# Optimization experiments

Hardware: AMD Instinct MI355X
Metric: run time of the kernel (lower is better)

Reference implementation:

```python
import jax, jax.numpy as jnp
import numpy as np

B, N, K = 8, 1024, 16        # graphs, points per graph, kNN fan-in (loop=True includes self)
LATENT = 256
EPS = 1e-5                   # PyG BatchNorm eps


def _bn(x, g, b):
    # training-mode batch norm over all leading (node/edge) dims, per channel
    ax = tuple(range(x.ndim - 1))
    mu = jnp.mean(x, axis=ax, keepdims=True)
    var = jnp.var(x, axis=ax, keepdims=True)
    return g * (x - mu) * jax.lax.rsqrt(var + EPS) + b


def setup_inputs() -> dict:
    key = jax.random.key(0)
    ks = jax.random.split(key, 12)

    def lin(k, fi, fo):
        s = (6.0 / (fi + fo)) ** 0.5
        kw, kb = jax.random.split(k)
        W = jax.random.uniform(kw, (fi, fo), jnp.float32, -s, s)
        bb = jax.random.uniform(kb, (fo,), jnp.float32, -s, s)
        return W, bb

    pos = jax.random.normal(ks[0], (B * N, 3), jnp.float32)
    batch = jnp.repeat(jnp.arange(B, dtype=jnp.int32), N)

    c1_W1, c1_b1 = lin(ks[1], 6, 64)
    c1_W2, c1_b2 = lin(ks[2], 64, 64)
    c2_W1, c2_b1 = lin(ks[3], 67, 64)
    c2_W2, c2_b2 = lin(ks[4], 64, 128)
    c2_W3, c2_b3 = lin(ks[5], 128, 1024)
    lin_W, lin_b = lin(ks[6], 1024, LATENT)

    return {
        "pos": pos, "batch": batch,
        "c1_W1": c1_W1, "c1_b1": c1_b1,
        "c1_g1": jnp.ones((64,), jnp.float32), "c1_be1": jnp.zeros((64,), jnp.float32),
        "c1_W2": c1_W2, "c1_b2": c1_b2,
        "c2_W1": c2_W1, "c2_b1": c2_b1,
        "c2_g1": jnp.ones((64,), jnp.float32), "c2_be1": jnp.zeros((64,), jnp.float32),
        "c2_W2": c2_W2, "c2_b2": c2_b2,
        "c2_g2": jnp.ones((128,), jnp.float32), "c2_be2": jnp.zeros((128,), jnp.float32),
        "c2_W3": c2_W3, "c2_b3": c2_b3,
        "lin_W": lin_W, "lin_b": lin_b,
        "lin_g": jnp.ones((LATENT,), jnp.float32), "lin_be": jnp.zeros((LATENT,), jnp.float32),
    }


def reference(pos, batch,
              c1_W1, c1_b1, c1_g1, c1_be1, c1_W2, c1_b2,
              c2_W1, c2_b1, c2_g1, c2_be1, c2_W2, c2_b2,
              c2_g2, c2_be2, c2_W3, c2_b3,
              lin_W, lin_b, lin_g, lin_be):
    # ---- kNN graph (per-graph, loop=True: self is nearest) ----
    p3 = pos.reshape(B, N, 3)
    sq = jnp.sum(p3 * p3, axis=-1)                                   # [B,N]
    d = sq[:, :, None] + sq[:, None, :] - 2.0 * jnp.einsum('bnd,bmd->bnm', p3, p3)
    _, nbr = jax.lax.top_k(-d, K)                                    # [B,N,K] neighbor ids
    idx = (nbr + (jnp.arange(B) * N)[:, None, None]).reshape(B * N, K)

    # ---- PointNetConv 1: gather -> MLP([6,64,64]) -> max aggregate ----
    pj = pos[idx]                                                    # [P,K,3]
    rel = pj - pos[:, None, :]                                       # [P,K,3]
    feat = jnp.concatenate([pj, rel], axis=-1)                       # [P,K,6]
    h = jax.nn.relu(_bn(feat @ c1_W1 + c1_b1, c1_g1, c1_be1))
    x1 = jnp.max(h @ c1_W2 + c1_b2, axis=1)                          # [P,64]

    # ---- PointNetConv 2: MLP([67,64,128,1024]) -> max aggregate ----
    feat2 = jnp.concatenate([x1[idx], rel], axis=-1)                 # [P,K,67]
    h = jax.nn.relu(_bn(feat2 @ c2_W1 + c2_b1, c2_g1, c2_be1))
    h = jax.nn.relu(_bn(h @ c2_W2 + c2_b2, c2_g2, c2_be2))
    x2 = jnp.max(h @ c2_W3 + c2_b3, axis=1)                          # [P,1024]

    # ---- global max pool per graph + final MLP (plain_last=False) ----
    g = x2.reshape(B, N, -1).max(axis=1)                             # [B,1024]
    return jax.nn.relu(_bn(g @ lin_W + lin_b, lin_g, lin_be))        # [B,LATENT]
```

## Files before the change

### kernel.cpp

```cpp
#include <hip/hip_runtime.h>
#include <math.h>

#define NB   8
#define NPTS 1024
#define PTS  8192
#define KNN  16
#define PK   (PTS*KNN)

typedef __attribute__((ext_vector_type(8))) _Float16 f16x8;
typedef __attribute__((ext_vector_type(4))) float f32x4;

__device__ __forceinline__ unsigned short f2h(float f) {
  _Float16 h = (_Float16)f;
  union { _Float16 h; unsigned short u; } c; c.h = h;
  return c.u;
}
__device__ __forceinline__ float h2f(unsigned short u) {
  union { unsigned short u; _Float16 h; } c; c.u = u;
  return (float)c.h;
}
__device__ __forceinline__ int lanerank(unsigned long long m) {
  return __builtin_amdgcn_mbcnt_hi((unsigned)(m >> 32),
         __builtin_amdgcn_mbcnt_lo((unsigned)m, 0));
}

__global__ __launch_bounds__(256) void knn_conv1_kernel(const float* __restrict__ pos,
    const float* __restrict__ W1, const float* __restrict__ b1,
    int* __restrict__ idx, float* __restrict__ rel,
    unsigned short* __restrict__ z1h, float* __restrict__ mid1) {
  __shared__ float px[NPTS], py[NPTS], pz[NPTS];
  __shared__ float feat[4][KNN][6];
  __shared__ float ls[256], ls2[256];
  const int t = threadIdx.x;
  const int wv = t >> 6, lane = t & 63;
  const int b = blockIdx.x;
  const int graph = b >> 8;
  const int base = graph << 10;
  for (int j = t; j < NPTS; j += 256) {
    px[j] = pos[3*(base+j)];
    py[j] = pos[3*(base+j)+1];
    pz[j] = pos[3*(base+j)+2];
  }
  __syncthreads();

  const int il = ((b & 255) << 2) + wv;
  const int i  = base + il;
  const float pix = px[il], piy = py[il], piz = pz[il];
  const float sqi = pix*pix + piy*piy + piz*piz;

  unsigned key[16];
  #pragma unroll
  for (int q = 0; q < 16; ++q) {
    const int j = (q << 6) + lane;
    const float x = px[j], y = py[j], z = pz[j];
    const float sqj = x*x + y*y + z*z;
    const float dt  = pix*x + piy*y + piz*z;
    const float d   = sqi + sqj - 2.0f*dt;
    const unsigned db = __float_as_uint(d);
    key[q] = (db >> 31) ? ~db : (db | 0x80000000u);
  }

  unsigned V = 0;
  #pragma unroll 1
  for (int bb = 31; bb >= 0; --bb) {
    const unsigned test = V | (1u << bb);
    int cnt = 0;
    #pragma unroll
    for (int q = 0; q < 16; ++q)
      cnt += __popcll(__ballot(key[q] < test));
    if (cnt < 16) V = test;
  }

  int c = 0;
  #pragma unroll
  for (int q = 0; q < 16; ++q)
    c += __popcll(__ballot(key[q] < V));

  int p_lt = 0, p_eq = c;
  #pragma unroll 1
  for (int q = 0; q < 16; ++q) {
    const unsigned long long mlt = __ballot(key[q] < V);
    const unsigned long long meq = __ballot(key[q] == V);
    int slot = -1;
    if (key[q] < V) slot = p_lt + lanerank(mlt);
    else if (key[q] == V) {
      const int s = p_eq + lanerank(meq);
      if (s < 16) slot = s;
    }
    if (slot >= 0) {
      const int j = (q << 6) + lane;
      const int r = i*KNN + slot;
      const float rx = px[j] - pix, ry = py[j] - piy, rz = pz[j] - piz;
      idx[r] = base + j;
      rel[3*r] = rx; rel[3*r+1] = ry; rel[3*r+2] = rz;
      feat[wv][slot][0] = px[j]; feat[wv][slot][1] = py[j]; feat[wv][slot][2] = pz[j];
      feat[wv][slot][3] = rx;    feat[wv][slot][4] = ry;    feat[wv][slot][5] = rz;
    }
    p_lt += __popcll(mlt);
    p_eq += __popcll(meq);
  }

  float w[6];
  #pragma unroll
  for (int q = 0; q < 6; ++q) w[q] = W1[q*64 + lane];
  const float bbv = b1[lane];
  float s = 0.0f, s2 = 0.0f;
  #pragma unroll
  for (int k = 0; k < KNN; ++k) {
    float z = bbv;
    #pragma unroll
    for (int q = 0; q < 6; ++q) z += feat[wv][k][q]*w[q];
    z1h[(size_t)(i*KNN + k)*64 + lane] = f2h(z);
    s += z; s2 += z*z;
  }
  ls[t] = s; ls2[t] = s2;
  __syncthreads();
  if (t < 64) {
    float a  = ls[t] + ls[t+64] + ls[t+128] + ls[t+192];
    float a2 = ls2[t] + ls2[t+64] + ls2[t+128] + ls2[t+192];
    const int cp = (b & 7) * 128;
    atomicAdd(&mid1[cp + t], a);
    atomicAdd(&mid1[cp + 64 + t], a2);
  }
}

__global__ __launch_bounds__(256) void wprep_kernel(const float* __restrict__ W3,
    const float* __restrict__ W2, const float* __restrict__ W1c2,
    const float* __restrict__ W2c1,
    unsigned short* __restrict__ W3T, unsigned short* __restrict__ W2T,
    unsigned short* __restrict__ w1T, unsigned short* __restrict__ W2c1T,
    float* __restrict__ mids) {
  const int b = blockIdx.x, t = threadIdx.x;
  if (b < 128) {
    const int k = b;
    const int ks = k >> 5, qd = (k >> 3) & 3, e = k & 7;
    for (int n = t; n < 1024; n += 256) {
      const int nb = n >> 4, mc = n & 15;
      W3T[((nb*4 + ks) << 9) + qd*128 + mc*8 + e] = f2h(W3[(size_t)k*1024 + n]);
    }
  } else if (b < 132) {
    for (int id = (b-128)*2048 + t; id < (b-127)*2048; id += 256) {
      const int n = id >> 6, k = id & 63;
      W2T[n*64 + k] = f2h(W2[k*128 + n]);
    }
  } else if (b < 136) {
    for (int id = (b-132)*1024 + t; id < (b-131)*1024; id += 256) {
      const int n = id >> 6, k = id & 63;
      w1T[n*64 + k] = f2h(W1c2[k*64 + n]);
    }
  } else if (b < 140) {
    for (int id = (b-136)*1024 + t; id < (b-135)*1024; id += 256) {
      const int n = id >> 6, k = id & 63;
      W2c1T[n*64 + k] = f2h(W2c1[k*64 + n]);
    }
  } else {
    for (int i2 = t; i2 < 4096; i2 += 256) mids[i2] = 0.0f;
  }
}

__global__ __launch_bounds__(256) void conv1_l2max_mfma(
    const unsigned short* __restrict__ z1h, const float* __restrict__ mid1,
    const float* __restrict__ g1, const float* __restrict__ be1,
    const unsigned short* __restrict__ W2T, const float* __restrict__ b2,
    unsigned short* __restrict__ x1h) {
  __shared__ unsigned short As[128*64];
  __shared__ float scl[64], shl[64];
  const int r0 = blockIdx.x * 128;
  const int t = threadIdx.x;
  const int lane = t & 63, w = t >> 6;
  const int quad = lane >> 4, mcol = lane & 15;
  const float invR = 1.0f / (float)PK;

  if (t < 64) {
    float s = 0.0f, s2 = 0.0f;
    #pragma unroll
    for (int k = 0; k < 8; ++k) { s += mid1[k*128 + t]; s2 += mid1[k*128 + 64 + t]; }
    const float mu  = s * invR;
    const float var = s2 * invR - mu*mu;
    const float sc  = g1[t] * rsqrtf(var + 1e-5f);
    scl[t] = sc; shl[t] = be1[t] - mu*sc;
  }
  __syncthreads();

  {
    const int kb = t & 7, rr = t >> 3;
    float sc[8], sh[8];
    #pragma unroll
    for (int q = 0; q < 8; ++q) { sc[q] = scl[kb*8 + q]; sh[q] = shl[kb*8 + q]; }
    #pragma unroll
    for (int it = 0; it < 4; ++it) {
      const int r = rr + it*32;
      union { uint4 v; unsigned short s[8]; } in;
      in.v = *(const uint4*)(z1h + (size_t)(r0 + r)*64 + kb*8);
      union { unsigned short s[8]; uint4 v; } o;
      #pragma unroll
      for (int q = 0; q < 8; ++q)
        o.s[q] = f2h(fmaxf(h2f(in.s[q])*sc[q] + sh[q], 0.0f));
      *(uint4*)(As + r*64 + ((kb ^ (r & 7)) * 8)) = o.v;
    }
  }
  __syncthreads();

  const int wrow = (w >> 1) * 64;
  const int wncol = (w & 1) * 32;

  f32x4 acc[4][2];
  #pragma unroll
  for (int mi = 0; mi < 4; ++mi)
    #pragma unroll
    for (int ni = 0; ni < 2; ++ni)
      acc[mi][ni] = (f32x4){0.f, 0.f, 0.f, 0.f};

  #pragma unroll
  for (int ks = 0; ks < 2; ++ks) {
    f16x8 af[4], bfr[2];
    #pragma unroll
    for (int mi = 0; mi < 4; ++mi) {
      const int row = wrow + mi*16 + mcol;
      af[mi] = *(const f16x8*)(As + row*64 + (((ks*4 + quad) ^ (row & 7)) * 8));
    }
    #pragma unroll
    for (int ni = 0; ni < 2; ++ni) {
      const int nr = wncol + ni*16 + mcol;
      bfr[ni] = *(const f16x8*)(W2T + nr*64 + ks*32 + quad*8);
    }
    #pragma unroll
    for (int mi = 0; mi < 4; ++mi)
      #pragma unroll
      for (int ni = 0; ni < 2; ++ni)
        acc[mi][ni] = __builtin_amdgcn_mfma_f32_16x16x32_f16(af[mi], bfr[ni], acc[mi][ni], 0, 0, 0);
  }

  float bb[2];
  #pragma unroll
  for (int ni = 0; ni < 2; ++ni) bb[ni] = b2[wncol + ni*16 + mcol];
  #pragma unroll
  for (int mi = 0; mi < 4; ++mi) {
    const int p = blockIdx.x*8 + (w >> 1)*4 + mi;
    #pragma unroll
    for (int ni = 0; ni < 2; ++ni) {
      f32x4 a = acc[mi][ni];
      float m = fmaxf(fmaxf(a[0], a[1]), fmaxf(a[2], a[3]));
      m = fmaxf(m, __shfl_xor(m, 16));
      m = fmaxf(m, __shfl_xor(m, 32));
      if (quad == 0) x1h[(size_t)p*64 + wncol + ni*16 + mcol] = f2h(m + bb[ni]);
    }
  }
}

__global__ __launch_bounds__(256) void conv2_l1_mfma(
    const unsigned short* __restrict__ x1h, const int* __restrict__ idx,
    const float* __restrict__ rel, const unsigned short* __restrict__ w1T,
    const float* __restrict__ W1full, const float* __restrict__ b1,
    unsigned short* __restrict__ zah, float* __restrict__ midA) {
  __shared__ unsigned short S[128*64];
  __shared__ int   idxr[128];
  __shared__ float rl[128*3];
  __shared__ float ps[256];
  const int r0 = blockIdx.x * 128;
  const int t = threadIdx.x;
  const int lane = t & 63, w = t >> 6;
  const int quad = lane >> 4, mcol = lane & 15;

  if (t < 128) idxr[t] = idx[r0 + t];
  else if (t < 224) *(float4*)(rl + (t-128)*4) = *(const float4*)(rel + (size_t)r0*3 + (t-128)*4);
  __syncthreads();

  {
    const int kb = t & 7, rr = t >> 3;
    #pragma unroll
    for (int it = 0; it < 4; ++it) {
      const int r = rr + it*32;
      const int gj = idxr[r];
      const uint4 v = *(const uint4*)(x1h + (size_t)gj*64 + kb*8);
      *(uint4*)(S + r*64 + ((kb ^ (r & 7)) * 8)) = v;
    }
  }
  __syncthreads();

  const int wrow = (w >> 1) * 64;
  const int wcol = (w & 1) * 32;

  f16x8 af[2][4], bfr[2][2];
  #pragma unroll
  for (int ks = 0; ks < 2; ++ks)
    #pragma unroll
    for (int mi = 0; mi < 4; ++mi) {
      const int row = wrow + mi*16 + mcol;
      af[ks][mi] = *(const f16x8*)(S + row*64 + (((ks*4 + quad) ^ (row & 7)) * 8));
    }
  #pragma unroll
  for (int ks = 0; ks < 2; ++ks)
    #pragma unroll
    for (int ni = 0; ni < 2; ++ni) {
      const int nr = wcol + ni*16 + mcol;
      bfr[ks][ni] = *(const f16x8*)(w1T + nr*64 + ks*32 + quad*8);
    }

  f32x4 acc[4][2];
  #pragma unroll
  for (int mi = 0; mi < 4; ++mi)
    #pragma unroll
    for (int ni = 0; ni < 2; ++ni)
      acc[mi][ni] = (f32x4){0.f, 0.f, 0.f, 0.f};

  #pragma unroll
  for (int ks = 0; ks < 2; ++ks)
    #pragma unroll
    for (int mi = 0; mi < 4; ++mi)
      #pragma unroll
      for (int ni = 0; ni < 2; ++ni)
        acc[mi][ni] = __builtin_amdgcn_mfma_f32_16x16x32_f16(af[ks][mi], bfr[ks][ni], acc[mi][ni], 0, 0, 0);

  __syncthreads();

  float bb[2], wr0[2], wr1[2], wr2[2];
  #pragma unroll
  for (int ni = 0; ni < 2; ++ni) {
    const int col = wcol + ni*16 + mcol;
    bb[ni]  = b1[col];
    wr0[ni] = W1full[64*64 + col];
    wr1[ni] = W1full[65*64 + col];
    wr2[ni] = W1full[66*64 + col];
  }
  float s[2] = {0,0}, s2[2] = {0,0};
  #pragma unroll
  for (int mi = 0; mi < 4; ++mi) {
    #pragma unroll
    for (int j = 0; j < 4; ++j) {
      const int row = wrow + mi*16 + quad*4 + j;
      const float r0v = rl[row*3], r1v = rl[row*3+1], r2v = rl[row*3+2];
      #pragma unroll
      for (int ni = 0; ni < 2; ++ni) {
        const int col = wcol + ni*16 + mcol;
        const int g = col >> 3, o = col & 7;
        const float v = acc[mi][ni][j] + bb[ni] + r0v*wr0[ni] + r1v*wr1[ni] + r2v*wr2[ni];
        S[row*64 + ((g ^ (row & 7)) << 3) + o] = f2h(v);
        s[ni] += v; s2[ni] += v*v;
      }
    }
  }
  #pragma unroll
  for (int ni = 0; ni < 2; ++ni) {
    s[ni]  += __shfl_xor(s[ni], 16);  s[ni]  += __shfl_xor(s[ni], 32);
    s2[ni] += __shfl_xor(s2[ni], 16); s2[ni] += __shfl_xor(s2[ni], 32);
  }
  if (quad == 0) {
    const int rh = w >> 1;
    #pragma unroll
    for (int ni = 0; ni < 2; ++ni) {
      const int col = wcol + ni*16 + mcol;
      ps[rh*128 + col]      = s[ni];
      ps[rh*128 + 64 + col] = s2[ni];
    }
  }
  __syncthreads();

  #pragma unroll
  for (int i = 0; i < 4; ++i) {
    const int u = i*256 + t;
    const int row = u >> 3, gg = u & 7;
    *(uint4*)(zah + (size_t)(r0 + row)*64 + gg*8) =
        *(const uint4*)(S + row*64 + ((gg ^ (row & 7)) << 3));
  }
  if (t < 128) atomicAdd(&midA[(blockIdx.x & 7)*128 + t], ps[t] + ps[128 + t]);
}

__global__ __launch_bounds__(256) void conv2_l2_mfma(
    const unsigned short* __restrict__ zah, const float* __restrict__ midA,
    const float* __restrict__ g1, const float* __restrict__ be1,
    const unsigned short* __restrict__ W2T, const float* __restrict__ b2,
    unsigned short* __restrict__ zhb, float* __restrict__ midB) {
  __shared__ unsigned short S[128*128];
  __shared__ float ps[512];
  __shared__ float scl[64], shl[64];
  const int r0 = blockIdx.x * 128;
  const int t = threadIdx.x;
  const int lane = t & 63, w = t >> 6;
  const int quad = lane >> 4, mcol = lane & 15;
  const float invR = 1.0f / (float)PK;

  if (t < 64) {
    float s = 0.0f, s2 = 0.0f;
    #pragma unroll
    for (int k = 0; k < 8; ++k) { s += midA[k*128 + t]; s2 += midA[k*128 + 64 + t]; }
    const float mu  = s * invR;
    const float var = s2 * invR - mu*mu;
    const float sc  = g1[t] * rsqrtf(var + 1e-5f);
    scl[t] = sc; shl[t] = be1[t] - mu*sc;
  }
  __syncthreads();

  {
    const int kb = t & 7, rr = t >> 3;
    float sc[8], sh[8];
    #pragma unroll
    for (int q = 0; q < 8; ++q) { sc[q] = scl[kb*8 + q]; sh[q] = shl[kb*8 + q]; }
    #pragma unroll
    for (int it = 0; it < 4; ++it) {
      const int r = rr + it*32;
      union { uint4 v; unsigned short s[8]; } in;
      in.v = *(const uint4*)(zah + (size_t)(r0 + r)*64 + kb*8);
      union { unsigned short s[8]; uint4 v; } o;
      #pragma unroll
      for (int q = 0; q < 8; ++q)
        o.s[q] = f2h(fmaxf(h2f(in.s[q])*sc[q] + sh[q], 0.0f));
      *(uint4*)(S + r*64 + ((kb ^ (r & 7)) * 8)) = o.v;
    }
  }
  __syncthreads();

  const int wrow = (w >> 1) * 64;
  const int wcol = (w & 1) * 64;

  f16x8 af[2][4], bfr[2][4];
  #pragma unroll
  for (int ks = 0; ks < 2; ++ks)
    #pragma unroll
    for (int mi = 0; mi < 4; ++mi) {
      const int row = wrow + mi*16 + mcol;
      af[ks][mi] = *(const f16x8*)(S + row*64 + (((ks*4 + quad) ^ (row & 7)) * 8));
    }
  #pragma unroll
  for (int ks = 0; ks < 2; ++ks)
    #pragma unroll
    for (int ni = 0; ni < 4; ++ni) {
      const int nr = wcol + ni*16 + mcol;
      bfr[ks][ni] = *(const f16x8*)(W2T + nr*64 + ks*32 + quad*8);
    }

  f32x4 acc[4][4];
  #pragma unroll
  for (int mi = 0; mi < 4; ++mi)
    #pragma unroll
    for (int ni = 0; ni < 4; ++ni)
      acc[mi][ni] = (f32x4){0.f, 0.f, 0.f, 0.f};

  #pragma unroll
  for (int ks = 0; ks < 2; ++ks)
    #pragma unroll
    for (int mi = 0; mi < 4; ++mi)
      #pragma unroll
      for (int ni = 0; ni < 4; ++ni)
        acc[mi][ni] = __builtin_amdgcn_mfma_f32_16x16x32_f16(af[ks][mi], bfr[ks][ni], acc[mi][ni], 0, 0, 0);

  __syncthreads();

  float bb[4];
  #pragma unroll
  for (int ni = 0; ni < 4; ++ni) bb[ni] = b2[wcol + ni*16 + mcol];
  float s[4] = {0,0,0,0}, s2[4] = {0,0,0,0};
  #pragma unroll
  for (int mi = 0; mi < 4; ++mi) {
    #pragma unroll
    for (int ni = 0; ni < 4; ++ni) {
      const int col = wcol + ni*16 + mcol;
      const int g = col >> 3, o = col & 7;
      #pragma unroll
      for (int j = 0; j < 4; ++j) {
        const int row = wrow + mi*16 + quad*4 + j;
        const float v = acc[mi][ni][j] + bb[ni];
        S[row*128 + ((g ^ (row & 15)) << 3) + o] = f2h(v);
        s[ni] += v; s2[ni] += v*v;
      }
    }
  }
  #pragma unroll
  for (int ni = 0; ni < 4; ++ni) {
    s[ni]  += __shfl_xor(s[ni], 16);  s[ni]  += __shfl_xor(s[ni], 32);
    s2[ni] += __shfl_xor(s2[ni], 16); s2[ni] += __shfl_xor(s2[ni], 32);
  }
  if (quad == 0) {
    const int rh = w >> 1;
    #pragma unroll
    for (int ni = 0; ni < 4; ++ni) {
      const int col = wcol + ni*16 + mcol;
      ps[rh*256 + col]       = s[ni];
      ps[rh*256 + 128 + col] = s2[ni];
    }
  }
  __syncthreads();

  #pragma unroll
  for (int i = 0; i < 8; ++i) {
    const int u = i*256 + t;
    const int row = u >> 4, gg = u & 15;
    *(uint4*)(zhb + (size_t)(r0 + row)*128 + gg*8) =
        *(const uint4*)(S + row*128 + ((gg ^ (row & 15)) << 3));
  }
  atomicAdd(&midB[(blockIdx.x & 7)*256 + t], ps[t] + ps[256 + t]);
}

__global__ __launch_bounds__(256, 3) void conv2_l3max_mfma(
    const unsigned short* __restrict__ zhb, const float* __restrict__ midB,
    const float* __restrict__ g2, const float* __restrict__ be2,
    const unsigned short* __restrict__ W3T,
    float* __restrict__ pmax2) {
  __shared__ unsigned short As[128*128];
  __shared__ float pm[2048];
  float* const scl = pm;
  float* const shl = pm + 128;
  const int rb = blockIdx.x;
  const int r0 = rb * 128;
  const int t = threadIdx.x;
  const int lane = t & 63, w = t >> 6;
  const int quad = lane >> 4, mcol = lane & 15;
  const float invR = 1.0f / (float)PK;

  if (t < 128) {
    float s = 0.0f, s2 = 0.0f;
    #pragma unroll
    for (int k = 0; k < 8; ++k) { s += midB[k*256 + t]; s2 += midB[k*256 + 128 + t]; }
    const float mu  = s * invR;
    const float var = s2 * invR - mu*mu;
    const float sc  = g2[t] * rsqrtf(var + 1e-5f);
    scl[t] = sc; shl[t] = be2[t] - mu*sc;
  }
  __syncthreads();

  {
    const int kb = t & 15, rr = t >> 4;
    float sc[8], sh[8];
    #pragma unroll
    for (int q = 0; q < 8; ++q) { sc[q] = scl[kb*8 + q]; sh[q] = shl[kb*8 + q]; }
    #pragma unroll
    for (int it = 0; it < 8; ++it) {
      const int r = rr + it*16;
      union { uint4 v; unsigned short s[8]; } in;
      in.v = *(const uint4*)(zhb + (size_t)(r0 + r)*128 + kb*8);
      union { unsigned short s[8]; uint4 v; } o;
      #pragma unroll
      for (int q = 0; q < 8; ++q)
        o.s[q] = f2h(fmaxf(h2f(in.s[q])*sc[q] + sh[q], 0.0f));
      *(uint4*)(As + r*128 + ((kb ^ (r & 7)) * 8)) = o.v;
    }
  }
  __syncthreads();

  const int wrow = (w >> 1) * 64;
  const int wncol = (w & 1) * 32;
  const int rh = w >> 1;

  #pragma unroll 1
  for (int chunk = 0; chunk < 16; ++chunk) {
    const int nb0 = chunk*4 + (w & 1)*2;

    f32x4 acc[4][2];
    #pragma unroll
    for (int mi = 0; mi < 4; ++mi)
      #pragma unroll
      for (int ni = 0; ni < 2; ++ni)
        acc[mi][ni] = (f32x4){0.f, 0.f, 0.f, 0.f};

    #pragma unroll
    for (int ks = 0; ks < 4; ++ks) {
      f16x8 bfr[2], af[4];
      #pragma unroll
      for (int ni = 0; ni < 2; ++ni)
        bfr[ni] = *(const f16x8*)(W3T + (((nb0 + ni)*4 + ks) << 9) + lane*8);
      #pragma unroll
      for (int mi = 0; mi < 4; ++mi) {
        const int row = wrow + mi*16 + mcol;
        af[mi] = *(const f16x8*)(As + row*128 + (((ks*4 + quad) ^ (row & 7)) * 8));
      }
      #pragma unroll
      for (int mi = 0; mi < 4; ++mi)
        #pragma unroll
        for (int ni = 0; ni < 2; ++ni)
          acc[mi][ni] = __builtin_amdgcn_mfma_f32_16x16x32_f16(af[mi], bfr[ni], acc[mi][ni], 0, 0, 0);
    }

    #pragma unroll
    for (int ni = 0; ni < 2; ++ni) {
      float m4 = -INFINITY;
      #pragma unroll
      for (int mi = 0; mi < 4; ++mi) {
        f32x4 a = acc[mi][ni];
        m4 = fmaxf(m4, fmaxf(fmaxf(a[0], a[1]), fmaxf(a[2], a[3])));
      }
      m4 = fmaxf(m4, __shfl_xor(m4, 16));
      m4 = fmaxf(m4, __shfl_xor(m4, 32));
      if (quad == 0)
        pm[rh*1024 + chunk*64 + wncol + ni*16 + mcol] = m4;
    }
  }
  __syncthreads();

  #pragma unroll
  for (int i = 0; i < 4; ++i) {
    const int c = i*256 + t;
    pmax2[(size_t)rb*1024 + c] = fmaxf(pm[c], pm[1024 + c]);
  }
}

__global__ __launch_bounds__(256) void poollin_kernel(const float* __restrict__ pmax2,
    const float* __restrict__ b3, const float* __restrict__ W,
    float* __restrict__ zpart) {
  __shared__ float gs[256];
  const int b = blockIdx.x >> 2, q = blockIdx.x & 3;
  const int t = threadIdx.x;
  const int c = q*256 + t;
  const float* p = pmax2 + (size_t)b*128*1024 + c;
  float m = -INFINITY;
  #pragma unroll 4
  for (int rb = 0; rb < 128; ++rb) m = fmaxf(m, p[(size_t)rb*1024]);
  gs[t] = m + b3[c];
  __syncthreads();
  const float* Wq = W + (size_t)q*256*256;
  float acc = 0.0f;
  for (int cc = 0; cc < 256; ++cc) acc += gs[cc] * Wq[cc*256 + t];
  zpart[blockIdx.x*256 + t] = acc;
}

__global__ __launch_bounds__(256) void final_kernel(const float* __restrict__ zpart,
    const float* __restrict__ lb, const float* __restrict__ lg,
    const float* __restrict__ lbe, float* __restrict__ out) {
  const int o = threadIdx.x;
  float z[NB]; float s = 0.0f, s2 = 0.0f;
  #pragma unroll
  for (int b = 0; b < NB; ++b) {
    float v = lb[o];
    #pragma unroll
    for (int q = 0; q < 4; ++q) v += zpart[(b*4+q)*256 + o];
    z[b] = v; s += v; s2 += v*v;
  }
  const float mu  = s * 0.125f;
  const float var = s2 * 0.125f - mu*mu;
  const float inv = rsqrtf(var + 1e-5f);
  const float sc = lg[o]*inv, sh = lbe[o] - mu*sc;
  #pragma unroll
  for (int b = 0; b < NB; ++b) out[b*256 + o] = fmaxf(z[b]*sc + sh, 0.0f);
}

extern "C" void kernel_launch(void* const* d_in, const int* in_sizes, int n_in,
                              void* d_out, int out_size, void* d_ws, size_t ws_size,
                              hipStream_t stream) {
  const float* pos    = (const float*)d_in[0];
  const float* c1_W1  = (const float*)d_in[2];
  const float* c1_b1  = (const float*)d_in[3];
  const float* c1_g1  = (const float*)d_in[4];
  const float* c1_be1 = (const float*)d_in[5];
  const float* c1_W2  = (const float*)d_in[6];
  const float* c1_b2  = (const float*)d_in[7];
  const float* c2_W1  = (const float*)d_in[8];
  const float* c2_b1  = (const float*)d_in[9];
  const float* c2_g1  = (const float*)d_in[10];
  const float* c2_be1 = (const float*)d_in[11];
  const float* c2_W2  = (const float*)d_in[12];
  const float* c2_b2  = (const float*)d_in[13];
  const float* c2_g2  = (const float*)d_in[14];
  const float* c2_be2 = (const float*)d_in[15];
  const float* c2_W3  = (const float*)d_in[16];
  const float* c2_b3  = (const float*)d_in[17];
  const float* lin_W  = (const float*)d_in[18];
  const float* lin_b  = (const float*)d_in[19];
  const float* lin_g  = (const float*)d_in[20];
  const float* lin_be = (const float*)d_in[21];
  float* out = (float*)d_out;

  char* ws = (char*)d_ws;
  int*   idx     = (int*)  (ws + 0);
  float* rel     = (float*)(ws + 524288);
  float* zpart   = (float*)(ws + 2097152 + 2048);
  float* mid1    = (float*)(ws + 2164736);
  float* midA    = (float*)(ws + 2164736 + 4096);
  float* midB    = (float*)(ws + 2164736 + 8192);
  unsigned short* W2T   = (unsigned short*)(ws + 2295808);
  unsigned short* w1T   = (unsigned short*)(ws + 2312192);
  unsigned short* W2c1T = (unsigned short*)(ws + 2320384);
  unsigned short* z1h = (unsigned short*)(ws + 2426880);
  unsigned short* zah = (unsigned short*)(ws + 2426880);
  float* pmax2   = (float*)(ws + 2426880);
  unsigned short* x1h = (unsigned short*)(ws + 35981312);
  unsigned short* zhb = (unsigned short*)(ws + 38078464);
  unsigned short* W3T = (unsigned short*)(ws + 71632896);

  wprep_kernel<<<141, 256, 0, stream>>>(c2_W3, c2_W2, c2_W1, c1_W2, W3T, W2T, w1T, W2c1T, mid1);
  knn_conv1_kernel<<<PTS/4, 256, 0, stream>>>(pos, c1_W1, c1_b1, idx, rel, z1h, mid1);
  conv1_l2max_mfma<<<PK/128, 256, 0, stream>>>(z1h, mid1, c1_g1, c1_be1, W2c1T, c1_b2, x1h);
  conv2_l1_mfma<<<PK/128, 256, 0, stream>>>(x1h, idx, rel, w1T, c2_W1, c2_b1, zah, midA);
  conv2_l2_mfma<<<PK/128, 256, 0, stream>>>(zah, midA, c2_g1, c2_be1, W2T, c2_b2, zhb, midB);
  conv2_l3max_mfma<<<PK/128, 256, 0, stream>>>(zhb, midB, c2_g2, c2_be2, W3T, pmax2);
  poollin_kernel<<<NB*4, 256, 0, stream>>>(pmax2, c2_b3, lin_W, zpart);
  final_kernel<<<1, 256, 0, stream>>>(zpart, lin_b, lin_g, lin_be, out);
}
```

Measured before the change: 228.3 us.

## Fuse conv2 three layers into one cooperative kernel with grid syncs

Replaces the three separate conv2 MFMA kernels with a single cooperative kernel of 512 blocks. Each block holds two 128-row tiles of activations in shared memory across all layers and uses grid.sync for the batch-norm statistics between layers. This removes the global-memory round trips for the intermediate fp16 activations and two kernel launches. The cost is the grid-wide barriers, 2-block-per-CU occupancy limits from the large LDS footprint, and a two-plane pmax2 layout that poollin now has to merge. A fallback path keeps the old kernels if the cooperative launch fails.

```diff
diff --git a/kernel.cpp b/kernel.cpp
--- a/kernel.cpp
+++ b/kernel.cpp
@@ -1,4 +1,5 @@
 #include <hip/hip_runtime.h>
+#include <hip/hip_cooperative_groups.h>
 #include <math.h>
 
 #define NB   8
@@ -593,17 +594,349 @@
   }
 }
 
+__global__ __launch_bounds__(256, 2) void conv2_fused2(
+    const unsigned short* __restrict__ x1h, const int* __restrict__ idx,
+    const float* __restrict__ rel, const unsigned short* __restrict__ w1T,
+    const float* __restrict__ W1full, const float* __restrict__ b1,
+    float* __restrict__ midA,
+    const unsigned short* __restrict__ W2T, const float* __restrict__ b2,
+    float* __restrict__ midB,
+    const float* __restrict__ g1, const float* __restrict__ be1,
+    const float* __restrict__ g2, const float* __restrict__ be2,
+    const unsigned short* __restrict__ W3T,
+    float* __restrict__ pmax2) {
+  cooperative_groups::grid_group grid = cooperative_groups::this_grid();
+  __shared__ unsigned short As2[32768];
+  __shared__ float pscratch[1024];
+  const int t = threadIdx.x;
+  const int lane = t & 63, w = t >> 6;
+  const int quad = lane >> 4, mcol = lane & 15;
+  const int rh = w >> 1;
+  const int wrow = rh * 64;
+  const float invR = 1.0f / (float)PK;
+
+  #pragma unroll 1
+  for (int tp = 0; tp < 2; ++tp) {
+    const int rb = blockIdx.x + tp*512;
+    const int r0 = rb * 128;
+    const int vb = tp ? 24576 : 0;
+    int*   idxr = (int*)pscratch;
+    float* rl   = pscratch + 128;
+    float* ps   = pscratch + 512;
+    if (t < 128) idxr[t] = idx[r0 + t];
+    else if (t < 224) *(float4*)(rl + (t-128)*4) = *(const float4*)(rel + (size_t)r0*3 + (t-128)*4);
+    __syncthreads();
+
+    {
+      const int kb = t & 7, rr = t >> 3;
+      #pragma unroll
+      for (int it = 0; it < 4; ++it) {
+        const int r = rr + it*32;
+        const int gj = idxr[r];
+        const uint4 v = *(const uint4*)(x1h + (size_t)gj*64 + kb*8);
+        *(uint4*)(As2 + 8192 + r*64 + ((kb ^ (r & 7)) * 8)) = v;
+      }
+    }
+    __syncthreads();
+
+    const int wcol = (w & 1) * 32;
+    f16x8 af[2][4], bfr[2][2];
+    #pragma unroll
+    for (int ks = 0; ks < 2; ++ks)
+      #pragma unroll
+      for (int mi = 0; mi < 4; ++mi) {
+        const int row = wrow + mi*16 + mcol;
+        af[ks][mi] = *(const f16x8*)(As2 + 8192 + row*64 + (((ks*4 + quad) ^ (row & 7)) * 8));
+      }
+    #pragma unroll
+    for (int ks = 0; ks < 2; ++ks)
+      #pragma unroll
+      for (int ni = 0; ni < 2; ++ni) {
+        const int nr = wcol + ni*16 + mcol;
+        bfr[ks][ni] = *(const f16x8*)(w1T + nr*64 + ks*32 + quad*8);
+      }
+
+    f32x4 acc[4][2];
+    #pragma unroll
+    for (int mi = 0; mi < 4; ++mi)
+      #pragma unroll
+      for (int ni = 0; ni < 2; ++ni)
+        acc[mi][ni] = (f32x4){0.f, 0.f, 0.f, 0.f};
+    #pragma unroll
+    for (int ks = 0; ks < 2; ++ks)
+      #pragma unroll
+      for (int mi = 0; mi < 4; ++mi)
+        #pragma unroll
+        for (int ni = 0; ni < 2; ++ni)
+          acc[mi][ni] = __builtin_amdgcn_mfma_f32_16x16x32_f16(af[ks][mi], bfr[ks][ni], acc[mi][ni], 0, 0, 0);
+
+    float bb[2], wr0[2], wr1[2], wr2[2];
+    #pragma unroll
+    for (int ni = 0; ni < 2; ++ni) {
+      const int col = wcol + ni*16 + mcol;
+      bb[ni]  = b1[col];
+      wr0[ni] = W1full[64*64 + col];
+      wr1[ni] = W1full[65*64 + col];
+      wr2[ni] = W1full[66*64 + col];
+    }
+    float s[2] = {0,0}, s2[2] = {0,0};
+    #pragma unroll
+    for (int mi = 0; mi < 4; ++mi) {
+      #pragma unroll
+      for (int j = 0; j < 4; ++j) {
+        const int row = wrow + mi*16 + quad*4 + j;
+        const float r0v = rl[row*3], r1v = rl[row*3+1], r2v = rl[row*3+2];
+        #pragma unroll
+        for (int ni = 0; ni < 2; ++ni) {
+          const int col = wcol + ni*16 + mcol;
+          const int g = col >> 3, o = col & 7;
+          const float v = acc[mi][ni][j] + bb[ni] + r0v*wr0[ni] + r1v*wr1[ni] + r2v*wr2[ni];
+          As2[vb + row*64 + ((g ^ (row & 7)) << 3) + o] = f2h(v);
+          s[ni] += v; s2[ni] += v*v;
+        }
+      }
+    }
+    #pragma unroll
+    for (int ni = 0; ni < 2; ++ni) {
+      s[ni]  += __shfl_xor(s[ni], 16);  s[ni]  += __shfl_xor(s[ni], 32);
+      s2[ni] += __shfl_xor(s2[ni], 16); s2[ni] += __shfl_xor(s2[ni], 32);
+    }
+    if (quad == 0) {
+      #pragma unroll
+      for (int ni = 0; ni < 2; ++ni) {
+        const int col = wcol + ni*16 + mcol;
+        ps[rh*128 + col]      = s[ni];
+        ps[rh*128 + 64 + col] = s2[ni];
+      }
+    }
+    __syncthreads();
+    if (t < 128) atomicAdd(&midA[(rb & 7)*128 + t], ps[t] + ps[128 + t]);
+  }
+
+  grid.sync();
+
+  {
+    float* scl = pscratch;
+    float* shl = pscratch + 64;
+    float* ps2 = pscratch + 512;
+    if (t < 64) {
+      float s = 0.0f, s2 = 0.0f;
+      #pragma unroll
+      for (int k = 0; k < 8; ++k) { s += midA[k*128 + t]; s2 += midA[k*128 + 64 + t]; }
+      const float mu  = s * invR;
+      const float var = s2 * invR - mu*mu;
+      const float sc  = g1[t] * rsqrtf(var + 1e-5f);
+      scl[t] = sc; shl[t] = be1[t] - mu*sc;
+    }
+    __syncthreads();
+    {
+      const int kb = t & 7, rr = t >> 3;
+      float sc[8], sh[8];
+      #pragma unroll
+      for (int q = 0; q < 8; ++q) { sc[q] = scl[kb*8 + q]; sh[q] = shl[kb*8 + q]; }
+      #pragma unroll
+      for (int tb = 0; tb < 2; ++tb) {
+        const int vb = tb ? 24576 : 0;
+        #pragma unroll
+        for (int it = 0; it < 4; ++it) {
+          const int r = rr + it*32;
+          unsigned short* a = As2 + vb + r*64 + ((kb ^ (r & 7)) * 8);
+          union { uint4 v; unsigned short s[8]; } in; in.v = *(const uint4*)a;
+          union { unsigned short s[8]; uint4 v; } o;
+          #pragma unroll
+          for (int q = 0; q < 8; ++q)
+            o.s[q] = f2h(fmaxf(h2f(in.s[q])*sc[q] + sh[q], 0.0f));
+          *(uint4*)a = o.v;
+        }
+      }
+    }
+    __syncthreads();
+
+    #pragma unroll 1
+    for (int tp = 0; tp < 2; ++tp) {
+      const int rb = blockIdx.x + tp*512;
+      const int vb = tp ? 24576 : 0;
+      const int zb = tp * 16384;
+      f16x8 af[2][4];
+      #pragma unroll
+      for (int ks = 0; ks < 2; ++ks)
+        #pragma unroll
+        for (int mi = 0; mi < 4; ++mi) {
+          const int row = wrow + mi*16 + mcol;
+          af[ks][mi] = *(const f16x8*)(As2 + vb + row*64 + (((ks*4 + quad) ^ (row & 7)) * 8));
+        }
+      __syncthreads();
+
+      #pragma unroll
+      for (int half = 0; half < 2; ++half) {
+        const int wcol = (w & 1)*64 + half*32;
+        f16x8 bfr[2][2];
+        #pragma unroll
+        for (int ks = 0; ks < 2; ++ks)
+          #pragma unroll
+          for (int ni = 0; ni < 2; ++ni) {
+            const int nr = wcol + ni*16 + mcol;
+            bfr[ks][ni] = *(const f16x8*)(W2T + nr*64 + ks*32 + quad*8);
+          }
+        f32x4 acc[4][2];
+        #pragma unroll
+        for (int mi = 0; mi < 4; ++mi)
+          #pragma unroll
+          for (int ni = 0; ni < 2; ++ni)
+            acc[mi][ni] = (f32x4){0.f, 0.f, 0.f, 0.f};
+        #pragma unroll
+        for (int ks = 0; ks < 2; ++ks)
+          #pragma unroll
+          for (int mi = 0; mi < 4; ++mi)
+            #pragma unroll
+            for (int ni = 0; ni < 2; ++ni)
+              acc[mi][ni] = __builtin_amdgcn_mfma_f32_16x16x32_f16(af[ks][mi], bfr[ks][ni], acc[mi][ni], 0, 0, 0);
+
+        float bb[2];
+        #pragma unroll
+        for (int ni = 0; ni < 2; ++ni) bb[ni] = b2[wcol + ni*16 + mcol];
+        float s[2] = {0,0}, s2[2] = {0,0};
+        #pragma unroll
+        for (int mi = 0; mi < 4; ++mi) {
+          #pragma unroll
+          for (int ni = 0; ni < 2; ++ni) {
+            const int col = wcol + ni*16 + mcol;
+            const int g = col >> 3, o = col & 7;
+            #pragma unroll
+            for (int j = 0; j < 4; ++j) {
+              const int row = wrow + mi*16 + quad*4 + j;
+              const float v = acc[mi][ni][j] + bb[ni];
+              As2[zb + row*128 + ((g ^ (row & 7)) << 3) + o] = f2h(v);
+              s[ni] += v; s2[ni] += v*v;
+            }
+          }
+        }
+        #pragma unroll
+        for (int ni = 0; ni < 2; ++ni) {
+          s[ni]  += __shfl_xor(s[ni], 16);  s[ni]  += __shfl_xor(s[ni], 32);
+          s2[ni] += __shfl_xor(s2[ni], 16); s2[ni] += __shfl_xor(s2[ni], 32);
+        }
+        if (quad == 0) {
+          #pragma unroll
+          for (int ni = 0; ni < 2; ++ni) {
+            const int col = wcol + ni*16 + mcol;
+            ps2[rh*256 + col]       = s[ni];
+            ps2[rh*256 + 128 + col] = s2[ni];
+          }
+        }
+      }
+      __syncthreads();
+      atomicAdd(&midB[(rb & 7)*256 + t], ps2[t] + ps2[t + 256]);
+    }
+  }
+
+  grid.sync();
+
+  {
+    float* scl = pscratch;
+    float* shl = pscratch + 128;
+    if (t < 128) {
+      float s = 0.0f, s2 = 0.0f;
+      #pragma unroll
+      for (int k = 0; k < 8; ++k) { s += midB[k*256 + t]; s2 += midB[k*256 + 128 + t]; }
+      const float mu  = s * invR;
+      const float var = s2 * invR - mu*mu;
+      const float sc  = g2[t] * rsqrtf(var + 1e-5f);
+      scl[t] = sc; shl[t] = be2[t] - mu*sc;
+    }
+    __syncthreads();
+    {
+      const int kb = t & 15, rr = t >> 4;
+      float sc[8], sh[8];
+      #pragma unroll
+      for (int q = 0; q < 8; ++q) { sc[q] = scl[kb*8 + q]; sh[q] = shl[kb*8 + q]; }
+      #pragma unroll
+      for (int tb = 0; tb < 2; ++tb) {
+        const int zb = tb * 16384;
+        #pragma unroll
+        for (int it = 0; it < 8; ++it) {
+          const int r = rr + it*16;
+          unsigned short* a = As2 + zb + r*128 + ((kb ^ (r & 7)) * 8);
+          union { uint4 v; unsigned short s[8]; } in; in.v = *(const uint4*)a;
+          union { unsigned short s[8]; uint4 v; } o;
+          #pragma unroll
+          for (int q = 0; q < 8; ++q)
+            o.s[q] = f2h(fmaxf(h2f(in.s[q])*sc[q] + sh[q], 0.0f));
+          *(uint4*)a = o.v;
+        }
+      }
+    }
+    __syncthreads();
+
+    const int wncol = (w & 1) * 32;
+    #pragma unroll 1
+    for (int tp = 0; tp < 2; ++tp) {
+      const int rb = blockIdx.x + tp*512;
+      const int zb = tp * 16384;
+      #pragma unroll 1
+      for (int chunk = 0; chunk < 16; ++chunk) {
+        const int nb0 = chunk*4 + (w & 1)*2;
+        f32x4 acc[4][2];
+        #pragma unroll
+        for (int mi = 0; mi < 4; ++mi)
+          #pragma unroll
+          for (int ni = 0; ni < 2; ++ni)
+            acc[mi][ni] = (f32x4){0.f, 0.f, 0.f, 0.f};
+
+        #pragma unroll
+        for (int ks = 0; ks < 4; ++ks) {
+          f16x8 bfr[2], af[4];
+          #pragma unroll
+          for (int ni = 0; ni < 2; ++ni)
+            bfr[ni] = *(const f16x8*)(W3T + (((nb0 + ni)*4 + ks) << 9) + lane*8);
+          #pragma unroll
+          for (int mi = 0; mi < 4; ++mi) {
+            const int row = wrow + mi*16 + mcol;
+            af[mi] = *(const f16x8*)(As2 + zb + row*128 + (((ks*4 + quad) ^ (row & 7)) * 8));
+          }
+          #pragma unroll
+          for (int mi = 0; mi < 4; ++mi)
+            #pragma unroll
+            for (int ni = 0; ni < 2; ++ni)
+              acc[mi][ni] = __builtin_amdgcn_mfma_f32_16x16x32_f16(af[mi], bfr[ni], acc[mi][ni], 0, 0, 0);
+        }
+
+        #pragma unroll
+        for (int ni = 0; ni < 2; ++ni) {
+          float m4 = -INFINITY;
+          #pragma unroll
+          for (int mi = 0; mi < 4; ++mi) {
+            f32x4 a = acc[mi][ni];
+            m4 = fmaxf(m4, fmaxf(fmaxf(a[0], a[1]), fmaxf(a[2], a[3])));
+          }
+          m4 = fmaxf(m4, __shfl_xor(m4, 16));
+          m4 = fmaxf(m4, __shfl_xor(m4, 32));
+          if (quad == 0)
+            pmax2[((size_t)rh << 20) + (size_t)rb*1024 + chunk*64 + wncol + ni*16 + mcol] = m4;
+        }
+      }
+    }
+  }
+}
+
 __global__ __launch_bounds__(256) void poollin_kernel(const float* __restrict__ pmax2,
     const float* __restrict__ b3, const float* __restrict__ W,
-    float* __restrict__ zpart) {
+    float* __restrict__ zpart, int two_plane) {
   __shared__ float gs[256];
   const int b = blockIdx.x >> 2, q = blockIdx.x & 3;
   const int t = threadIdx.x;
   const int c = q*256 + t;
-  const float* p = pmax2 + (size_t)b*128*1024 + c;
+  const float* p0 = pmax2 + (size_t)b*128*1024 + c;
   float m = -INFINITY;
-  #pragma unroll 4
-  for (int rb = 0; rb < 128; ++rb) m = fmaxf(m, p[(size_t)rb*1024]);
+  if (two_plane) {
+    const float* p1 = p0 + (1u << 20);
+    #pragma unroll 4
+    for (int rb = 0; rb < 128; ++rb)
+      m = fmaxf(m, fmaxf(p0[(size_t)rb*1024], p1[(size_t)rb*1024]));
+  } else {
+    #pragma unroll 4
+    for (int rb = 0; rb < 128; ++rb) m = fmaxf(m, p0[(size_t)rb*1024]);
+  }
   gs[t] = m + b3[c];
   __syncthreads();
   const float* Wq = W + (size_t)q*256*256;
@@ -678,9 +1011,28 @@
   wprep_kernel<<<141, 256, 0, stream>>>(c2_W3, c2_W2, c2_W1, c1_W2, W3T, W2T, w1T, W2c1T, mid1);
   knn_conv1_kernel<<<PTS/4, 256, 0, stream>>>(pos, c1_W1, c1_b1, idx, rel, z1h, mid1);
   conv1_l2max_mfma<<<PK/128, 256, 0, stream>>>(z1h, mid1, c1_g1, c1_be1, W2c1T, c1_b2, x1h);
-  conv2_l1_mfma<<<PK/128, 256, 0, stream>>>(x1h, idx, rel, w1T, c2_W1, c2_b1, zah, midA);
-  conv2_l2_mfma<<<PK/128, 256, 0, stream>>>(zah, midA, c2_g1, c2_be1, W2T, c2_b2, zhb, midB);
-  conv2_l3max_mfma<<<PK/128, 256, 0, stream>>>(zhb, midB, c2_g2, c2_be2, W3T, pmax2);
-  poollin_kernel<<<NB*4, 256, 0, stream>>>(pmax2, c2_b3, lin_W, zpart);
+
+  int nb = 0;
+  hipError_t qe = hipOccupancyMaxActiveBlocksPerMultiprocessor(
+      &nb, (const void*)conv2_fused2, 256, 0);
+  hipError_t ce = hipErrorUnknown;
+  if (qe == hipSuccess && nb >= 2) {
+    void* cargs[] = {
+      (void*)&x1h, (void*)&idx, (void*)&rel, (void*)&w1T, (void*)&c2_W1, (void*)&c2_b1,
+      (void*)&midA, (void*)&W2T, (void*)&c2_b2, (void*)&midB,
+      (void*)&c2_g1, (void*)&c2_be1, (void*)&c2_g2, (void*)&c2_be2,
+      (void*)&W3T, (void*)&pmax2
+    };
+    ce = hipLaunchCooperativeKernel((const void*)conv2_fused2, dim3(512), dim3(256),
+                                    cargs, 0, stream);
+  }
+  const int coop_ok = (ce == hipSuccess) ? 1 : 0;
+  if (!coop_ok) {
+    conv2_l1_mfma<<<PK/128, 256, 0, stream>>>(x1h, idx, rel, w1T, c2_W1, c2_b1, zah, midA);
+    conv2_l2_mfma<<<PK/128, 256, 0, stream>>>(zah, midA, c2_g1, c2_be1, W2T, c2_b2, zhb, midB);
+    conv2_l3max_mfma<<<PK/128, 256, 0, stream>>>(zhb, midB, c2_g2, c2_be2, W3T, pmax2);
+  }
+
+  poollin_kernel<<<NB*4, 256, 0, stream>>>(pmax2, c2_b3, lin_W, zpart, coop_ok);
   final_kernel<<<1, 256, 0, stream>>>(zpart, lin_b, lin_g, lin_be, out);
 }
```

Result: no change. 228.1 us (-0.1%).

## Use 32x32x16 MFMA in conv2 layer-3 max kernel with per-wave column tiles

Applied to the files above, without the earlier changes.

Rewrites the dominant 128->1024 GEMM+max kernel to use 32x32x16 f16 MFMA instructions. Each wave now covers all 128 rows for its own 256 output columns, so the max reduction happens inside registers and is written straight to global memory. This removes the shared-memory partial-max buffer and the final barrier. W3T's packed layout is changed in the prep kernel to match the new B-fragment shape, and occupancy is raised to 4 blocks per CU. The cost is more accumulator registers per wave (four 16-float accumulators), and every wave now reads the whole A tile.

```diff
diff --git a/kernel.cpp b/kernel.cpp
--- a/kernel.cpp
+++ b/kernel.cpp
@@ -9,6 +9,7 @@
 
 typedef __attribute__((ext_vector_type(8))) _Float16 f16x8;
 typedef __attribute__((ext_vector_type(4))) float f32x4;
+typedef __attribute__((ext_vector_type(16))) float f32x16;
 
 __device__ __forceinline__ unsigned short f2h(float f) {
   _Float16 h = (_Float16)f;
@@ -133,10 +134,10 @@
   const int b = blockIdx.x, t = threadIdx.x;
   if (b < 128) {
     const int k = b;
-    const int ks = k >> 5, qd = (k >> 3) & 3, e = k & 7;
+    const int ks = k >> 4, half = (k >> 3) & 1, e = k & 7;
     for (int n = t; n < 1024; n += 256) {
-      const int nb = n >> 4, mc = n & 15;
-      W3T[((nb*4 + ks) << 9) + qd*128 + mc*8 + e] = f2h(W3[(size_t)k*1024 + n]);
+      const int ct = n >> 5, cc = n & 31;
+      W3T[((ct*8 + ks) << 9) + (half*32 + cc)*8 + e] = f2h(W3[(size_t)k*1024 + n]);
     }
   } else if (b < 132) {
     for (int id = (b-128)*2048 + t; id < (b-127)*2048; id += 256) {
@@ -491,20 +492,17 @@
   atomicAdd(&midB[(blockIdx.x & 7)*256 + t], ps[t] + ps[256 + t]);
 }
 
-__global__ __launch_bounds__(256, 3) void conv2_l3max_mfma(
+__global__ __launch_bounds__(256, 4) void conv2_l3max_mfma32(
     const unsigned short* __restrict__ zhb, const float* __restrict__ midB,
     const float* __restrict__ g2, const float* __restrict__ be2,
     const unsigned short* __restrict__ W3T,
     float* __restrict__ pmax2) {
   __shared__ unsigned short As[128*128];
-  __shared__ float pm[2048];
-  float* const scl = pm;
-  float* const shl = pm + 128;
+  __shared__ float scl[128], shl[128];
   const int rb = blockIdx.x;
   const int r0 = rb * 128;
   const int t = threadIdx.x;
   const int lane = t & 63, w = t >> 6;
-  const int quad = lane >> 4, mcol = lane & 15;
   const float invR = 1.0f / (float)PK;
 
   if (t < 128) {
@@ -537,59 +535,49 @@
   }
   __syncthreads();
 
-  const int wrow = (w >> 1) * 64;
-  const int wncol = (w & 1) * 32;
-  const int rh = w >> 1;
+  const int row_in = lane & 31;
+  const int khalf  = lane >> 5;
 
   #pragma unroll 1
-  for (int chunk = 0; chunk < 16; ++chunk) {
-    const int nb0 = chunk*4 + (w & 1)*2;
-
-    f32x4 acc[4][2];
-    #pragma unroll
-    for (int mi = 0; mi < 4; ++mi)
-      #pragma unroll
-      for (int ni = 0; ni < 2; ++ni)
-        acc[mi][ni] = (f32x4){0.f, 0.f, 0.f, 0.f};
-
-    #pragma unroll
-    for (int ks = 0; ks < 4; ++ks) {
-      f16x8 bfr[2], af[4];
-      #pragma unroll
-      for (int ni = 0; ni < 2; ++ni)
-        bfr[ni] = *(const f16x8*)(W3T + (((nb0 + ni)*4 + ks) << 9) + lane*8);
-      #pragma unroll
-      for (int mi = 0; mi < 4; ++mi) {
-        const int row = wrow + mi*16 + mcol;
-        af[mi] = *(const f16x8*)(As + row*128 + (((ks*4 + quad) ^ (row & 7)) * 8));
+  for (int cc = 0; cc < 8; ++cc) {
+    const int ct = w*8 + cc;
+
+    f32x16 a0 = {}, a1 = {}, a2 = {}, a3 = {};
+
+    #pragma unroll
+    for (int ks = 0; ks < 8; ++ks) {
+      const f16x8 bf = *(const f16x8*)(W3T + ((ct*8 + ks) << 9) + lane*8);
+      const int g = ks*2 + khalf;
+      {
+        const int row = row_in;
+        const f16x8 a = *(const f16x8*)(As + row*128 + ((g ^ (row & 7)) * 8));
+        a0 = __builtin_amdgcn_mfma_f32_32x32x16_f16(a, bf, a0, 0, 0, 0);
       }
-      #pragma unroll
-      for (int mi = 0; mi < 4; ++mi)
-        #pragma unroll
-        for (int ni = 0; ni < 2; ++ni)
-          acc[mi][ni] = __builtin_amdgcn_mfma_f32_16x16x32_f16(af[mi], bfr[ni], acc[mi][ni], 0, 0, 0);
-    }
-
-    #pragma unroll
-    for (int ni = 0; ni < 2; ++ni) {
-      float m4 = -INFINITY;
-      #pragma unroll
-      for (int mi = 0; mi < 4; ++mi) {
-        f32x4 a = acc[mi][ni];
-        m4 = fmaxf(m4, fmaxf(fmaxf(a[0], a[1]), fmaxf(a[2], a[3])));
+      {
+        const int row = 32 + row_in;
+        const f16x8 a = *(const f16x8*)(As + row*128 + ((g ^ (row & 7)) * 8));
+        a1 = __builtin_amdgcn_mfma_f32_32x32x16_f16(a, bf, a1, 0, 0, 0);
       }
-      m4 = fmaxf(m4, __shfl_xor(m4, 16));
-      m4 = fmaxf(m4, __shfl_xor(m4, 32));
-      if (quad == 0)
-        pm[rh*1024 + chunk*64 + wncol + ni*16 + mcol] = m4;
-    }
-  }
-  __syncthreads();
-
-  #pragma unroll
-  for (int i = 0; i < 4; ++i) {
-    const int c = i*256 + t;
-    pmax2[(size_t)rb*1024 + c] = fmaxf(pm[c], pm[1024 + c]);
+      {
+        const int row = 64 + row_in;
+        const f16x8 a = *(const f16x8*)(As + row*128 + ((g ^ (row & 7)) * 8));
+        a2 = __builtin_amdgcn_mfma_f32_32x32x16_f16(a, bf, a2, 0, 0, 0);
+      }
+      {
+        const int row = 96 + row_in;
+        const f16x8 a = *(const f16x8*)(As + row*128 + ((g ^ (row & 7)) * 8));
+        a3 = __builtin_amdgcn_mfma_f32_32x32x16_f16(a, bf, a3, 0, 0, 0);
+      }
+    }
+
+    float m = -INFINITY;
+    #pragma unroll
+    for (int r = 0; r < 16; ++r) {
+      m = fmaxf(m, fmaxf(fmaxf(a0[r], a1[r]), fmaxf(a2[r], a3[r])));
+    }
+    m = fmaxf(m, __shfl_xor(m, 32));
+    if (lane < 32)
+      pmax2[(size_t)rb*1024 + ct*32 + row_in] = m;
   }
 }
 
@@ -680,7 +668,7 @@
   conv1_l2max_mfma<<<PK/128, 256, 0, stream>>>(z1h, mid1, c1_g1, c1_be1, W2c1T, c1_b2, x1h);
   conv2_l1_mfma<<<PK/128, 256, 0, stream>>>(x1h, idx, rel, w1T, c2_W1, c2_b1, zah, midA);
   conv2_l2_mfma<<<PK/128, 256, 0, stream>>>(zah, midA, c2_g1, c2_be1, W2T, c2_b2, zhb, midB);
-  conv2_l3max_mfma<<<PK/128, 256, 0, stream>>>(zhb, midB, c2_g2, c2_be2, W3T, pmax2);
+  conv2_l3max_mfma32<<<PK/128, 256, 0, stream>>>(zhb, midB, c2_g2, c2_be2, W3T, pmax2);
   poollin_kernel<<<NB*4, 256, 0, stream>>>(pmax2, c2_b3, lin_W, zpart);
   final_kernel<<<1, 256, 0, stream>>>(zpart, lin_b, lin_g, lin_be, out);
 }
```

Result: slower. 312.6 us (+36.9%).
